# Kernel optimization log

Measured on AMD Instinct MI355X. Metric: run time of the kernel, lower is better.

The kernel has to match this reference:

```python
import jax, jax.numpy as jnp
import numpy as np

N = 50000          # num member nodes == num provider nodes
E = 800000         # provider->member bipartite edges (avg degree 16)
IN_M = 128; IN_P = 128; HID = 128; HEADS = 4; LAT = 64
NEG = 0.2          # leaky_relu negative slope (PyG GATConv default)


def gat_conv(x, src, dst, W, a_src, a_dst, b, heads, ch):
    """PyG-style GATConv (eval mode, concat heads). x:[N,F], src/dst:[Etot]."""
    n = x.shape[0]
    h = (x @ W).reshape(n, heads, ch)                       # [N,H,C]
    s = jnp.sum(h * a_src, axis=-1)                         # [N,H]
    d = jnp.sum(h * a_dst, axis=-1)                         # [N,H]
    e = jax.nn.leaky_relu(s[src] + d[dst], NEG)             # [Etot,H]
    # segment softmax over edges grouped by destination node
    m = jax.ops.segment_max(e, dst, num_segments=n)
    p = jnp.exp(e - m[dst])
    z = jax.ops.segment_sum(p, dst, num_segments=n)
    alpha = p / (z[dst] + 1e-16)                            # [Etot,H]
    out = jax.ops.segment_sum(h[src] * alpha[..., None], dst, num_segments=n)
    return out.reshape(n, heads * ch) + b


def setup_inputs() -> dict:
    key = jax.random.key(0)
    ks = jax.random.split(key, 24)
    gl = lambda k, shape, fan: (jax.random.normal(k, shape, jnp.float32) / np.sqrt(fan).astype(np.float32))
    return {
        "x_member": jax.random.normal(ks[0], (N, IN_M), jnp.float32),
        "x_provider": jax.random.normal(ks[1], (N, IN_P), jnp.float32),
        "edge_index": jax.random.randint(ks[2], (2, E), 0, N),
        "W1_m": gl(ks[3], (IN_M, HID), IN_M),
        "a_src1_m": gl(ks[4], (HEADS, HID // HEADS), HID // HEADS),
        "a_dst1_m": gl(ks[5], (HEADS, HID // HEADS), HID // HEADS),
        "b1_m": jnp.zeros((HID,), jnp.float32),
        "W2_m": gl(ks[6], (HID, LAT), HID),
        "a_src2_m": gl(ks[7], (1, LAT), LAT),
        "a_dst2_m": gl(ks[8], (1, LAT), LAT),
        "b2_m": jnp.zeros((LAT,), jnp.float32),
        "W1_p": gl(ks[9], (IN_P, HID), IN_P),
        "a_src1_p": gl(ks[10], (HEADS, HID // HEADS), HID // HEADS),
        "a_dst1_p": gl(ks[11], (HEADS, HID // HEADS), HID // HEADS),
        "b1_p": jnp.zeros((HID,), jnp.float32),
        "W2_p": gl(ks[12], (HID, LAT), HID),
        "a_src2_p": gl(ks[13], (1, LAT), LAT),
        "a_dst2_p": gl(ks[14], (1, LAT), LAT),
        "b2_p": jnp.zeros((LAT,), jnp.float32),
        "Wd_m": gl(ks[15], (LAT, IN_M), LAT),
        "bd_m": jnp.zeros((IN_M,), jnp.float32),
        "Wd_p": gl(ks[16], (LAT, IN_P), LAT),
        "bd_p": jnp.zeros((IN_P,), jnp.float32),
    }


def reference(x_member, x_provider, edge_index,
              W1_m, a_src1_m, a_dst1_m, b1_m, W2_m, a_src2_m, a_dst2_m, b2_m,
              W1_p, a_src1_p, a_dst1_p, b1_p, W2_p, a_src2_p, a_dst2_p, b2_p,
              Wd_m, bd_m, Wd_p, bd_p):
    prov, memb = edge_index[0], edge_index[1]
    loop = jnp.arange(N)
    # member graph: self loops + (provider -> member); provider graph: reverse
    m_src = jnp.concatenate([loop, prov]); m_dst = jnp.concatenate([loop, memb])
    p_src = jnp.concatenate([loop, memb]); p_dst = jnp.concatenate([loop, prov])

    xm = jax.nn.elu(gat_conv(x_member, m_src, m_dst, W1_m, a_src1_m, a_dst1_m, b1_m, HEADS, HID // HEADS))
    z_m = gat_conv(xm, m_src, m_dst, W2_m, a_src2_m, a_dst2_m, b2_m, 1, LAT)

    xp = jax.nn.elu(gat_conv(x_provider, p_src, p_dst, W1_p, a_src1_p, a_dst1_p, b1_p, HEADS, HID // HEADS))
    z_p = gat_conv(xp, p_src, p_dst, W2_p, a_src2_p, a_dst2_p, b2_p, 1, LAT)

    x_hat_member = z_m @ Wd_m + bd_m
    x_hat_provider = z_p @ Wd_p + bd_p
    edge_logits = jnp.sum(z_p[prov] * z_m[memb], axis=1)
    return (x_hat_member, x_hat_provider, edge_logits)
```

## Files before the change

kernel.cpp:

```cpp
#include <hip/hip_runtime.h>
#include <hip/hip_fp16.h>
#include <stdint.h>

__device__ __forceinline__ unsigned int pack_h2(float a, float b) {
    return (unsigned int)__half_as_ushort(__float2half(a)) |
           ((unsigned int)__half_as_ushort(__float2half(b)) << 16);
}
__device__ __forceinline__ float4 cvt_h4(uint2 r) {
    __half2 h0 = *reinterpret_cast<__half2*>(&r.x);
    __half2 h1 = *reinterpret_cast<__half2*>(&r.y);
    float2 f0 = __half22float2(h0), f1 = __half22float2(h1);
    return make_float4(f0.x, f0.y, f1.x, f1.y);
}

template<int K, int COUT, bool ADD_BIAS, bool IN_HALF, bool OUT_HALF>
__global__ __launch_bounds__(256) void gemm_kernel(const void* __restrict__ X0,
                                                   const void* __restrict__ X1,
                                                   const float* __restrict__ W0,
                                                   const float* __restrict__ W1,
                                                   const float* __restrict__ b0,
                                                   const float* __restrict__ b1,
                                                   void* __restrict__ out0,
                                                   void* __restrict__ out1, int n)
{
    constexpr int KC   = 64;
    constexpr int CPT  = (COUT >= 128) ? 8 : 4;
    constexpr int TX   = COUT / CPT;
    constexpr int TY   = 256 / TX;
    constexpr int ROWS = TY * 4;

    __shared__ float Wl[KC * COUT];
    __shared__ float Xl[KC * ROWS];

    const int side = blockIdx.y;
    const void*  Xv   = side ? X1 : X0;
    const float* W    = side ? W1 : W0;
    const float* bias = side ? b1 : b0;
    void* outp        = side ? out1 : out0;

    const int tid  = threadIdx.x;
    const int row0 = blockIdx.x * ROWS;
    const int tx = tid % TX, ty = tid / TX;
    const int c0 = tx * CPT;

    float acc[4][CPT];
    #pragma unroll
    for (int i = 0; i < 4; ++i)
        #pragma unroll
        for (int j = 0; j < CPT; ++j) acc[i][j] = 0.f;

    for (int k0 = 0; k0 < K; k0 += KC) {
        for (int i = tid; i < KC * COUT / 4; i += 256) {
            int e0 = i * 4;
            int r = e0 / COUT, c = e0 - r * COUT;
            reinterpret_cast<float4*>(Wl)[i] =
                *reinterpret_cast<const float4*>(W + (size_t)(k0 + r) * COUT + c);
        }
        for (int i = tid; i < ROWS * KC / 4; i += 256) {
            int r = i / (KC / 4), c4 = i - r * (KC / 4);
            int gr = row0 + r;
            float4 v = make_float4(0.f, 0.f, 0.f, 0.f);
            if (gr < n) {
                if constexpr (IN_HALF) {
                    const __half* X = (const __half*)Xv;
                    v = cvt_h4(*reinterpret_cast<const uint2*>(X + (size_t)gr * K + k0 + c4 * 4));
                } else {
                    const float* X = (const float*)Xv;
                    v = *reinterpret_cast<const float4*>(X + (size_t)gr * K + k0 + c4 * 4);
                }
            }
            int cb = c4 * 4;
            Xl[(cb + 0) * ROWS + r] = v.x;
            Xl[(cb + 1) * ROWS + r] = v.y;
            Xl[(cb + 2) * ROWS + r] = v.z;
            Xl[(cb + 3) * ROWS + r] = v.w;
        }
        __syncthreads();

        #pragma unroll 16
        for (int kk = 0; kk < KC; ++kk) {
            float b[CPT];
            #pragma unroll
            for (int j = 0; j < CPT; ++j) b[j] = Wl[kk * COUT + c0 + j];
            float4 a4 = *reinterpret_cast<const float4*>(Xl + kk * ROWS + ty * 4);
            float a[4] = {a4.x, a4.y, a4.z, a4.w};
            #pragma unroll
            for (int i = 0; i < 4; ++i)
                #pragma unroll
                for (int j = 0; j < CPT; ++j)
                    acc[i][j] = fmaf(a[i], b[j], acc[i][j]);
        }
        __syncthreads();
    }

    #pragma unroll
    for (int i = 0; i < 4; ++i) {
        int gr = row0 + ty * 4 + i;
        if (gr < n) {
            float v[CPT];
            #pragma unroll
            for (int j = 0; j < CPT; ++j) {
                v[j] = acc[i][j];
                if constexpr (ADD_BIAS) v[j] += bias[c0 + j];
            }
            if constexpr (OUT_HALF) {
                __half* po = (__half*)outp + (size_t)gr * COUT + c0;
                if constexpr (CPT == 8) {
                    uint4 w;
                    w.x = pack_h2(v[0], v[1]); w.y = pack_h2(v[2], v[3]);
                    w.z = pack_h2(v[4], v[5]); w.w = pack_h2(v[6], v[7]);
                    *reinterpret_cast<uint4*>(po) = w;
                } else {
                    uint2 w;
                    w.x = pack_h2(v[0], v[1]); w.y = pack_h2(v[2], v[3]);
                    *reinterpret_cast<uint2*>(po) = w;
                }
            } else {
                float* po = (float*)outp + (size_t)gr * COUT + c0;
                #pragma unroll
                for (int j = 0; j < CPT; ++j) po[j] = v[j];
            }
        }
    }
}

template<int C, int H>
__global__ __launch_bounds__(256) void sd_kernel(const __half* __restrict__ hm,
                                                 const __half* __restrict__ hp,
                                                 const float* __restrict__ as_m,
                                                 const float* __restrict__ ad_m,
                                                 const float* __restrict__ as_p,
                                                 const float* __restrict__ ad_p,
                                                 float* __restrict__ s,
                                                 float* __restrict__ d, int N)
{
    constexpr int CH = C / H;
    int t = blockIdx.x * 256 + threadIdx.x;
    if (t >= 2 * N * H) return;
    int node = t / H, hh = t - (t / H) * H;
    int side = node >= N;
    int lN = node - (side ? N : 0);
    const __half* hfp = (side ? hp : hm) + (size_t)lN * C + hh * CH;
    const float* as = (side ? as_p : as_m) + hh * CH;
    const float* ad = (side ? ad_p : ad_m) + hh * CH;
    float av = 0.f, dv = 0.f;
    #pragma unroll
    for (int c = 0; c < CH; ++c) {
        float hv = __half2float(hfp[c]);
        av = fmaf(hv, as[c], av);
        dv = fmaf(hv, ad[c], dv);
    }
    s[t] = av; d[t] = dv;
}

#define BSH 7
#define BCAP 2560
#define CHUNK_E 4096

__global__ __launch_bounds__(256) void bucket_scatter_kernel(const int* __restrict__ prov,
                                                             const int* __restrict__ memb,
                                                             int* __restrict__ bcnt,
                                                             int2* __restrict__ bstore,
                                                             int e, int n, int nbuck)
{
    __shared__ int hist[1024];
    __shared__ int lbase[1024];
    const int tid = threadIdx.x;
    const int e0 = blockIdx.x * CHUNK_E;
    const int e1 = min(e, e0 + CHUNK_E);

    for (int i = tid; i < nbuck; i += 256) hist[i] = 0;
    __syncthreads();
    for (int t = e0 + tid; t < e1; t += 256) {
        int m = memb[t], p = prov[t];
        atomicAdd(&hist[m >> BSH], 1);
        atomicAdd(&hist[(n + p) >> BSH], 1);
    }
    __syncthreads();
    for (int i = tid; i < nbuck; i += 256) {
        int h = hist[i];
        lbase[i] = (h > 0) ? atomicAdd(&bcnt[i], h) : 0;
        hist[i] = 0;
    }
    __syncthreads();
    for (int t = e0 + tid; t < e1; t += 256) {
        int m = memb[t], p = prov[t];
        int b1 = m >> BSH;
        int pos1 = lbase[b1] + atomicAdd(&hist[b1], 1);
        if (pos1 < BCAP) bstore[(size_t)b1 * BCAP + pos1] = make_int2(m, p);
        int d2 = n + p;
        int b2 = d2 >> BSH;
        int pos2 = lbase[b2] + atomicAdd(&hist[b2], 1);
        if (pos2 < BCAP) bstore[(size_t)b2 * BCAP + pos2] = make_int2(d2, m);
    }
}

__global__ __launch_bounds__(1024) void bucket_scan_kernel(const int* __restrict__ bcnt,
                                                           int* __restrict__ bbase,
                                                           int* __restrict__ roff,
                                                           int nb, int n2)
{
    __shared__ int tmp[1024];
    int tid = threadIdx.x;
    int v = (tid < nb) ? min(bcnt[tid], BCAP) : 0;
    tmp[tid] = v; __syncthreads();
    for (int o = 1; o < 1024; o <<= 1) {
        int x = (tid >= o) ? tmp[tid - o] : 0;
        __syncthreads();
        tmp[tid] += x;
        __syncthreads();
    }
    bbase[tid] = tmp[tid] - v;
    if (tid == 0) roff[n2] = tmp[1023];
}

__global__ __launch_bounds__(256) void bucket_build_kernel(const int* __restrict__ bcnt,
                                                           const int* __restrict__ bbase,
                                                           const int2* __restrict__ bstore,
                                                           int* __restrict__ roff,
                                                           int* __restrict__ colA,
                                                           int n2)
{
    __shared__ int2 ent[BCAP];
    __shared__ int  colL[BCAP];
    __shared__ int  cnts[128], pref[128], curs[128];

    const int b = blockIdx.x, tid = threadIdx.x;
    const int node0 = b << BSH;
    const int cnt  = min(bcnt[b], BCAP);
    const int base = bbase[b];

    if (tid < 128) cnts[tid] = 0;
    __syncthreads();
    for (int i = tid; i < cnt; i += 256) {
        int2 v = bstore[(size_t)b * BCAP + i];
        ent[i] = v;
        atomicAdd(&cnts[v.x - node0], 1);
    }
    __syncthreads();
    if (tid < 128) pref[tid] = cnts[tid];
    __syncthreads();
    #pragma unroll
    for (int o = 1; o < 128; o <<= 1) {
        int x = 0;
        if (tid < 128 && tid >= o) x = pref[tid - o];
        __syncthreads();
        if (tid < 128) pref[tid] += x;
        __syncthreads();
    }
    if (tid < 128) {
        int node = node0 + tid;
        if (node < n2) roff[node] = base + pref[tid] - cnts[tid];
        curs[tid] = 0;
    }
    __syncthreads();
    for (int i = tid; i < cnt; i += 256) {
        int2 v = ent[i];
        int loc = v.x - node0;
        int slot = (pref[loc] - cnts[loc]) + atomicAdd(&curs[loc], 1);
        colL[slot] = v.y;
    }
    __syncthreads();
    for (int i = tid; i < cnt; i += 256) colA[base + i] = colL[i];
}

template<int H>
__device__ __forceinline__ float selH(const float* arr, int hd) {
    float v = arr[0];
    #pragma unroll
    for (int hh = 1; hh < H; ++hh) v = (hd == hh) ? arr[hh] : v;
    return v;
}

template<int C, int H, bool ELU, bool OUTH>
__device__ __forceinline__ void agg_one_fullwave(int iG, int lN, int lane,
                                                 const __half* __restrict__ hf,
                                                 const float* __restrict__ sarr,
                                                 const float* __restrict__ sb,
                                                 const float* __restrict__ darr,
                                                 const int* __restrict__ roff,
                                                 const int* __restrict__ col,
                                                 const float* __restrict__ bias,
                                                 void* __restrict__ out,
                                                 float* alsW, int* srcsW)
{
    constexpr int CH = C / H;
    constexpr int LR = C / 4;
    constexpr int EP = 64 / LR;
    const int start = roff[iG], end = roff[iG + 1];
    const int deg = end - start;

    float dh[H], es[H];
    #pragma unroll
    for (int hh = 0; hh < H; ++hh) dh[hh] = darr[(size_t)iG * H + hh];
    #pragma unroll
    for (int hh = 0; hh < H; ++hh) {
        float e = sarr[(size_t)iG * H + hh] + dh[hh];
        es[hh] = fmaxf(e, 0.2f * e);
    }

    if (deg <= 64) {
        int srcL = (lane < deg) ? col[start + lane] : 0;
        float pl[H], zh[H];
        if (lane < deg) {
            #pragma unroll
            for (int hh = 0; hh < H; ++hh) {
                float e = sb[(size_t)srcL * H + hh] + dh[hh];
                pl[hh] = __expf(fmaxf(e, 0.2f * e));
            }
        } else {
            #pragma unroll
            for (int hh = 0; hh < H; ++hh) pl[hh] = 0.f;
        }
        #pragma unroll
        for (int hh = 0; hh < H; ++hh) zh[hh] = pl[hh];
        #pragma unroll
        for (int hh = 0; hh < H; ++hh)
            for (int o = 32; o >= 1; o >>= 1)
                zh[hh] += __shfl_xor(zh[hh], o, 64);
        if (lane < deg) srcsW[lane] = srcL;
        float aself[H];
        #pragma unroll
        for (int hh = 0; hh < H; ++hh) {
            float se = __expf(es[hh]);
            float invz = 1.f / (zh[hh] + se + 1e-16f);
            aself[hh] = se * invz;
            if (lane < deg) alsW[hh * 65 + lane] = pl[hh] * invz;
        }
        asm volatile("s_waitcnt lgkmcnt(0)" ::: "memory");

        const int sub = lane / LR;
        const int q   = lane % LR;
        const int c0  = q * 4;
        const int hd  = c0 / CH;

        float4 acc = make_float4(0.f, 0.f, 0.f, 0.f);
        if (sub == 0) {
            float4 hv = cvt_h4(*reinterpret_cast<const uint2*>(hf + (size_t)lN * C + c0));
            float a = selH<H>(aself, hd);
            acc.x = a * hv.x; acc.y = a * hv.y; acc.z = a * hv.z; acc.w = a * hv.w;
        }
        const float* alsB = alsW + hd * 65;
        int t = sub;
#define GSTEP(U)                                                                     \
        while (t + (U - 1) * EP < deg) {                                             \
            int ss[U]; float aa[U]; uint2 rr[U];                                     \
            _Pragma("unroll")                                                        \
            for (int u = 0; u < U; ++u) { ss[u] = srcsW[t + u * EP]; aa[u] = alsB[t + u * EP]; } \
            _Pragma("unroll")                                                        \
            for (int u = 0; u < U; ++u)                                              \
                rr[u] = *reinterpret_cast<const uint2*>(hf + (size_t)ss[u] * C + c0); \
            _Pragma("unroll")                                                        \
            for (int u = 0; u < U; ++u) {                                            \
                float4 hv = cvt_h4(rr[u]);                                           \
                acc.x = fmaf(aa[u], hv.x, acc.x);                                    \
                acc.y = fmaf(aa[u], hv.y, acc.y);                                    \
                acc.z = fmaf(aa[u], hv.z, acc.z);                                    \
                acc.w = fmaf(aa[u], hv.w, acc.w);                                    \
            }                                                                        \
            t += U * EP;                                                             \
        }
        GSTEP(8)
        GSTEP(4)
        GSTEP(2)
        GSTEP(1)
#undef GSTEP
        #pragma unroll
        for (int o = LR; o < 64; o <<= 1) {
            acc.x += __shfl_xor(acc.x, o, 64);
            acc.y += __shfl_xor(acc.y, o, 64);
            acc.z += __shfl_xor(acc.z, o, 64);
            acc.w += __shfl_xor(acc.w, o, 64);
        }
        if (sub == 0) {
            float4 bv = *reinterpret_cast<const float4*>(bias + c0);
            float4 v = make_float4(acc.x + bv.x, acc.y + bv.y, acc.z + bv.z, acc.w + bv.w);
            if constexpr (ELU) {
                v.x = (v.x > 0.f) ? v.x : (__expf(v.x) - 1.f);
                v.y = (v.y > 0.f) ? v.y : (__expf(v.y) - 1.f);
                v.z = (v.z > 0.f) ? v.z : (__expf(v.z) - 1.f);
                v.w = (v.w > 0.f) ? v.w : (__expf(v.w) - 1.f);
            }
            if constexpr (OUTH) {
                uint2 w; w.x = pack_h2(v.x, v.y); w.y = pack_h2(v.z, v.w);
                *reinterpret_cast<uint2*>((__half*)out + (size_t)lN * C + c0) = w;
            } else {
                *reinterpret_cast<float4*>((float*)out + (size_t)lN * C + c0) = v;
            }
        }
        return;
    }

    float zh[H];
    #pragma unroll
    for (int hh = 0; hh < H; ++hh) zh[hh] = 0.f;
    for (int base = start; base < end; base += 64) {
        int idx = base + lane;
        if (idx < end) {
            int src = col[idx];
            #pragma unroll
            for (int hh = 0; hh < H; ++hh) {
                float e = sb[(size_t)src * H + hh] + dh[hh];
                e = fmaxf(e, 0.2f * e);
                zh[hh] += __expf(e);
            }
        }
    }
    #pragma unroll
    for (int hh = 0; hh < H; ++hh) {
        for (int o = 32; o >= 1; o >>= 1) zh[hh] += __shfl_xor(zh[hh], o, 64);
        zh[hh] += __expf(es[hh]);
    }

    constexpr int CPL = C / 64;
    const int cc0 = lane * CPL;
    const int hdl = cc0 / CH;
    const float invz = 1.f / (zh[hdl] + 1e-16f);
    const float d_l  = dh[hdl];

    float acc2[CPL];
    {
        float aself = __expf(es[hdl]) * invz;
        #pragma unroll
        for (int j = 0; j < CPL; ++j) acc2[j] = aself * __half2float(hf[(size_t)lN * C + cc0 + j]);
    }
    for (int base = start; base < end; base += 64) {
        int idx = base + lane;
        int srcL2 = (idx < end) ? col[idx] : 0;
        int cnt2 = min(64, end - base);
        for (int t = 0; t < cnt2; ++t) {
            int st = __shfl(srcL2, t, 64);
            float e = sb[(size_t)st * H + hdl] + d_l;
            e = fmaxf(e, 0.2f * e);
            float a = __expf(e) * invz;
            #pragma unroll
            for (int j = 0; j < CPL; ++j)
                acc2[j] = fmaf(a, __half2float(hf[(size_t)st * C + cc0 + j]), acc2[j]);
        }
    }
    #pragma unroll
    for (int j = 0; j < CPL; ++j) {
        int c = cc0 + j;
        float v = acc2[j] + bias[c];
        if constexpr (ELU) v = (v > 0.f) ? v : (__expf(v) - 1.f);
        if constexpr (OUTH) ((__half*)out)[(size_t)lN * C + c] = __float2half(v);
        else                ((float*)out)[(size_t)lN * C + c] = v;
    }
}

template<int C, int H, bool ELU, bool OUTH>
__global__ __launch_bounds__(256) void agg_kernel(const __half* __restrict__ hm,
                                                  const __half* __restrict__ hp,
                                                  const float* __restrict__ sarr,
                                                  const float* __restrict__ darr,
                                                  const int* __restrict__ roff,
                                                  const int* __restrict__ col,
                                                  const float* __restrict__ bias_m,
                                                  const float* __restrict__ bias_p,
                                                  void* __restrict__ out_m,
                                                  void* __restrict__ out_p, int N)
{
    constexpr int CH  = C / H;
    constexpr int LRd = C / 8;
    constexpr int EPd = 32 / LRd;
    constexpr int H33 = H * 33;
    constexpr int ALSZ = (2 * H33 > H * 65) ? 2 * H33 : H * 65;
    __shared__ float als[4][ALSZ];
    __shared__ int   srcs[4][64];

    const int n2 = 2 * N;
    const int wslot = threadIdx.x >> 6;
    const int wv    = (blockIdx.x * 256 + threadIdx.x) >> 6;
    const int lane  = threadIdx.x & 63;
    const int g = lane >> 5, l = lane & 31;
    const int i0 = wv * 2;
    if (i0 >= n2) return;

    const bool nval = (i0 + g) < n2;
    const int iN = nval ? (i0 + g) : (n2 - 1);
    const int side = (iN >= N) ? 1 : 0;
    const int lN = iN - side * N;
    const __half* hf = side ? hp : hm;
    const float* sb = sarr + (size_t)side * N * H;
    const float* biasS = side ? bias_p : bias_m;
    void* outS = side ? out_p : out_m;

    const int start = roff[iN], end = roff[iN + 1];
    const int deg = nval ? (end - start) : 0;
    const int degO = __shfl_xor(deg, 32, 64);
    const int degm = max(deg, degO);

    if (degm <= 32) {
        float dh[H], es[H];
        if constexpr (H == 4) {
            float4 dv = *reinterpret_cast<const float4*>(darr + (size_t)iN * 4);
            float4 sv = *reinterpret_cast<const float4*>(sarr + (size_t)iN * 4);
            dh[0] = dv.x; dh[1] = dv.y; dh[2] = dv.z; dh[3] = dv.w;
            float ev[4] = {sv.x + dv.x, sv.y + dv.y, sv.z + dv.z, sv.w + dv.w};
            #pragma unroll
            for (int hh = 0; hh < 4; ++hh) es[hh] = fmaxf(ev[hh], 0.2f * ev[hh]);
        } else {
            #pragma unroll
            for (int hh = 0; hh < H; ++hh) {
                dh[hh] = darr[(size_t)iN * H + hh];
                float e = sarr[(size_t)iN * H + hh] + dh[hh];
                es[hh] = fmaxf(e, 0.2f * e);
            }
        }

        int srcL = (l < deg) ? col[start + l] : 0;
        float pl[H];
        if (l < deg) {
            if constexpr (H == 4) {
                float4 sv = *reinterpret_cast<const float4*>(sb + (size_t)srcL * 4);
                float ee[4] = {sv.x + dh[0], sv.y + dh[1], sv.z + dh[2], sv.w + dh[3]};
                #pragma unroll
                for (int hh = 0; hh < 4; ++hh) pl[hh] = __expf(fmaxf(ee[hh], 0.2f * ee[hh]));
            } else {
                #pragma unroll
                for (int hh = 0; hh < H; ++hh) {
                    float e = sb[(size_t)srcL * H + hh] + dh[hh];
                    pl[hh] = __expf(fmaxf(e, 0.2f * e));
                }
            }
        } else {
            #pragma unroll
            for (int hh = 0; hh < H; ++hh) pl[hh] = 0.f;
        }
        float zh[H];
        #pragma unroll
        for (int hh = 0; hh < H; ++hh) zh[hh] = pl[hh];
        #pragma unroll
        for (int hh = 0; hh < H; ++hh)
            #pragma unroll
            for (int o = 16; o >= 1; o >>= 1)
                zh[hh] += __shfl_xor(zh[hh], o, 64);
        if (l < deg) srcs[wslot][g * 32 + l] = srcL;
        float aself[H];
        #pragma unroll
        for (int hh = 0; hh < H; ++hh) {
            float se = __expf(es[hh]);
            float invz = 1.f / (zh[hh] + se + 1e-16f);
            aself[hh] = se * invz;
            if (l < deg) als[wslot][g * H33 + hh * 33 + l] = pl[hh] * invz;
        }
        asm volatile("s_waitcnt lgkmcnt(0)" ::: "memory");

        const int sub = l / LRd;
        const int q   = l % LRd;
        const int c0  = q * 8;
        const int hd  = c0 / CH;

        float acc[8];
        #pragma unroll
        for (int j = 0; j < 8; ++j) acc[j] = 0.f;
        if (sub == 0) {
            uint4 r = *reinterpret_cast<const uint4*>(hf + (size_t)lN * C + c0);
            float4 lo = cvt_h4(make_uint2(r.x, r.y));
            float4 hi = cvt_h4(make_uint2(r.z, r.w));
            float a = selH<H>(aself, hd);
            acc[0] = a * lo.x; acc[1] = a * lo.y; acc[2] = a * lo.z; acc[3] = a * lo.w;
            acc[4] = a * hi.x; acc[5] = a * hi.y; acc[6] = a * hi.z; acc[7] = a * hi.w;
        }
        const int*   srcB = &srcs[wslot][g * 32];
        const float* alsB = &als[wslot][g * H33 + hd * 33];
        int t = sub;
#define GSTEP(U)                                                                     \
        while (t + (U - 1) * EPd < deg) {                                            \
            int ss[U]; float aa[U]; uint4 rr[U];                                     \
            _Pragma("unroll")                                                        \
            for (int u = 0; u < U; ++u) { ss[u] = srcB[t + u * EPd]; aa[u] = alsB[t + u * EPd]; } \
            _Pragma("unroll")                                                        \
            for (int u = 0; u < U; ++u)                                              \
                rr[u] = *reinterpret_cast<const uint4*>(hf + (size_t)ss[u] * C + c0); \
            _Pragma("unroll")                                                        \
            for (int u = 0; u < U; ++u) {                                            \
                float4 lo = cvt_h4(make_uint2(rr[u].x, rr[u].y));                    \
                float4 hi = cvt_h4(make_uint2(rr[u].z, rr[u].w));                    \
                acc[0] = fmaf(aa[u], lo.x, acc[0]);                                  \
                acc[1] = fmaf(aa[u], lo.y, acc[1]);                                  \
                acc[2] = fmaf(aa[u], lo.z, acc[2]);                                  \
                acc[3] = fmaf(aa[u], lo.w, acc[3]);                                  \
                acc[4] = fmaf(aa[u], hi.x, acc[4]);                                  \
                acc[5] = fmaf(aa[u], hi.y, acc[5]);                                  \
                acc[6] = fmaf(aa[u], hi.z, acc[6]);                                  \
                acc[7] = fmaf(aa[u], hi.w, acc[7]);                                  \
            }                                                                        \
            t += U * EPd;                                                            \
        }
        GSTEP(4)
        GSTEP(2)
        GSTEP(1)
#undef GSTEP
        #pragma unroll
        for (int o = LRd; o < 32; o <<= 1) {
            #pragma unroll
            for (int j = 0; j < 8; ++j) acc[j] += __shfl_xor(acc[j], o, 64);
        }
        if (sub == 0 && nval) {
            float4 b0 = *reinterpret_cast<const float4*>(biasS + c0);
            float4 b1 = *reinterpret_cast<const float4*>(biasS + c0 + 4);
            float v[8] = {acc[0] + b0.x, acc[1] + b0.y, acc[2] + b0.z, acc[3] + b0.w,
                          acc[4] + b1.x, acc[5] + b1.y, acc[6] + b1.z, acc[7] + b1.w};
            if constexpr (ELU) {
                #pragma unroll
                for (int j = 0; j < 8; ++j) v[j] = (v[j] > 0.f) ? v[j] : (__expf(v[j]) - 1.f);
            }
            if constexpr (OUTH) {
                uint4 w;
                w.x = pack_h2(v[0], v[1]); w.y = pack_h2(v[2], v[3]);
                w.z = pack_h2(v[4], v[5]); w.w = pack_h2(v[6], v[7]);
                *reinterpret_cast<uint4*>((__half*)outS + (size_t)lN * C + c0) = w;
            } else {
                float* po = (float*)outS + (size_t)lN * C + c0;
                *reinterpret_cast<float4*>(po)     = make_float4(v[0], v[1], v[2], v[3]);
                *reinterpret_cast<float4*>(po + 4) = make_float4(v[4], v[5], v[6], v[7]);
            }
        }
        return;
    }

    for (int nd = 0; nd < 2; ++nd) {
        int i = i0 + nd;
        if (i >= n2) break;
        int sd2 = (i >= N) ? 1 : 0;
        int ln2 = i - sd2 * N;
        agg_one_fullwave<C, H, ELU, OUTH>(i, ln2, lane,
                                          sd2 ? hp : hm,
                                          sarr, sarr + (size_t)sd2 * N * H, darr,
                                          roff, col,
                                          sd2 ? bias_p : bias_m,
                                          sd2 ? out_p : out_m,
                                          als[wslot], srcs[wslot]);
    }
}

__global__ __launch_bounds__(256) void logits_kernel(const float* __restrict__ zp,
                                                     const float* __restrict__ zm,
                                                     const int* __restrict__ prov,
                                                     const int* __restrict__ memb,
                                                     float* __restrict__ outv, int e)
{
    const int nw   = (gridDim.x * 256) >> 6;
    const int wv   = (blockIdx.x * 256 + threadIdx.x) >> 6;
    const int lane = threadIdx.x & 63;
    const int g = lane >> 4, q = lane & 15;
    for (int base = wv * 8; base < e; base += nw * 8) {
        int e1 = base + g, e2 = base + 4 + g;
        bool v1 = e1 < e, v2 = e2 < e;
        int i1 = v1 ? e1 : (e - 1), i2 = v2 ? e2 : (e - 1);
        int p1 = prov[i1], m1 = memb[i1];
        int p2 = prov[i2], m2 = memb[i2];
        float4 a1 = *reinterpret_cast<const float4*>(zp + (size_t)p1 * 64 + q * 4);
        float4 b1 = *reinterpret_cast<const float4*>(zm + (size_t)m1 * 64 + q * 4);
        float4 a2 = *reinterpret_cast<const float4*>(zp + (size_t)p2 * 64 + q * 4);
        float4 b2 = *reinterpret_cast<const float4*>(zm + (size_t)m2 * 64 + q * 4);
        float s1 = a1.x * b1.x + a1.y * b1.y + a1.z * b1.z + a1.w * b1.w;
        float s2 = a2.x * b2.x + a2.y * b2.y + a2.z * b2.z + a2.w * b2.w;
        #pragma unroll
        for (int o = 1; o < 16; o <<= 1) {
            s1 += __shfl_xor(s1, o, 64);
            s2 += __shfl_xor(s2, o, 64);
        }
        if (q == 0) {
            if (v1) outv[e1] = s1;
            if (v2) outv[e2] = s2;
        }
    }
}

extern "C" void kernel_launch(void* const* d_in, const int* in_sizes, int n_in,
                              void* d_out, int out_size, void* d_ws, size_t ws_size,
                              hipStream_t stream)
{
    const int N_ = in_sizes[0] / 128;
    const int E_ = in_sizes[2] / 2;

    const float* x_member   = (const float*)d_in[0];
    const float* x_provider = (const float*)d_in[1];
    const int*   prov = (const int*)d_in[2];
    const int*   memb = prov + E_;
    const float* W1_m = (const float*)d_in[3];
    const float* a_src1_m = (const float*)d_in[4];
    const float* a_dst1_m = (const float*)d_in[5];
    const float* b1_m = (const float*)d_in[6];
    const float* W2_m = (const float*)d_in[7];
    const float* a_src2_m = (const float*)d_in[8];
    const float* a_dst2_m = (const float*)d_in[9];
    const float* b2_m = (const float*)d_in[10];
    const float* W1_p = (const float*)d_in[11];
    const float* a_src1_p = (const float*)d_in[12];
    const float* a_dst1_p = (const float*)d_in[13];
    const float* b1_p = (const float*)d_in[14];
    const float* W2_p = (const float*)d_in[15];
    const float* a_src2_p = (const float*)d_in[16];
    const float* a_dst2_p = (const float*)d_in[17];
    const float* b2_p = (const float*)d_in[18];
    const float* Wd_m = (const float*)d_in[19];
    const float* bd_m = (const float*)d_in[20];
    const float* Wd_p = (const float*)d_in[21];
    const float* bd_p = (const float*)d_in[22];

    const int n2 = 2 * N_;
    const int NB = (n2 + 127) >> BSH;

    char* p = (char*)d_ws;
    auto alloc = [&](size_t bytes) { void* q = (void*)p; p += (bytes + 255) & ~(size_t)255; return q; };
    __half* h1m   = (__half*)alloc((size_t)N_ * 128 * 2);
    __half* h1p   = (__half*)alloc((size_t)N_ * 128 * 2);
    __half* xm16m = (__half*)alloc((size_t)N_ * 128 * 2);
    __half* xm16p = (__half*)alloc((size_t)N_ * 128 * 2);
    float* zm     = (float*)alloc((size_t)N_ * 64 * 4);
    float* zp     = (float*)alloc((size_t)N_ * 64 * 4);
    float* s1     = (float*)alloc((size_t)n2 * 4 * 4);
    float* d1     = (float*)alloc((size_t)n2 * 4 * 4);
    float* s2     = (float*)alloc((size_t)n2 * 4);
    float* d2     = (float*)alloc((size_t)n2 * 4);
    int*   bcnt   = (int*)alloc((size_t)NB * 4);
    int*   bbase  = (int*)alloc(1024 * 4);
    int*   roff2  = (int*)alloc((size_t)(n2 + 1) * 4);
    int*   colA   = (int*)alloc((size_t)2 * E_ * 4);
    __half* h2m = h1m;
    __half* h2p = h1p;
    int2*  bstore = (int2*)h1m;

    hipMemsetAsync(bcnt, 0, (size_t)NB * 4, stream);
    bucket_scatter_kernel<<<(E_ + CHUNK_E - 1) / CHUNK_E, 256, 0, stream>>>(prov, memb, bcnt, bstore, E_, N_, NB);
    bucket_scan_kernel<<<1, 1024, 0, stream>>>(bcnt, bbase, roff2, NB, n2);
    bucket_build_kernel<<<NB, 256, 0, stream>>>(bcnt, bbase, bstore, roff2, colA, n2);

    const dim3 gg((N_ + 63) / 64, 2);

    gemm_kernel<128, 128, false, false, true><<<gg, 256, 0, stream>>>(
        x_member, x_provider, W1_m, W1_p, nullptr, nullptr, h1m, h1p, N_);
    sd_kernel<128, 4><<<(n2 * 4 + 255) / 256, 256, 0, stream>>>(
        h1m, h1p, a_src1_m, a_dst1_m, a_src1_p, a_dst1_p, s1, d1, N_);
    agg_kernel<128, 4, true, true><<<(n2 + 7) / 8, 256, 0, stream>>>(
        h1m, h1p, s1, d1, roff2, colA, b1_m, b1_p, xm16m, xm16p, N_);

    gemm_kernel<128, 64, false, true, true><<<gg, 256, 0, stream>>>(
        xm16m, xm16p, W2_m, W2_p, nullptr, nullptr, h2m, h2p, N_);
    sd_kernel<64, 1><<<(n2 + 255) / 256, 256, 0, stream>>>(
        h2m, h2p, a_src2_m, a_dst2_m, a_src2_p, a_dst2_p, s2, d2, N_);
    agg_kernel<64, 1, false, false><<<(n2 + 7) / 8, 256, 0, stream>>>(
        h2m, h2p, s2, d2, roff2, colA, b2_m, b2_p, zm, zp, N_);

    float* out = (float*)d_out;
    gemm_kernel<64, 128, true, false, false><<<gg, 256, 0, stream>>>(
        zm, zp, Wd_m, Wd_p, bd_m, bd_p, out, out + (size_t)N_ * 128, N_);
    logits_kernel<<<2048, 256, 0, stream>>>(zp, zm, prov, memb, out + (size_t)N_ * 128 * 2, E_);
}
```

Baseline: 513.9 us.

## Fuse attention score dots into GEMM epilogue and store latent z in fp16

Computes the per-node source and destination attention scores inside the GEMM epilogue using a lane shuffle reduction, and removes the two separate sd_kernel launches along with their re-read of h. The second-layer aggregation now writes z in fp16, which the decoder GEMM and the edge logits kernel read with half-width loads. An 8-wide unrolled gather step is also added to the aggregation loop. The fp16 z lowers precision of the outputs and logits, and the epilogue adds shuffles to the GEMM.

```diff
diff --git a/kernel.cpp b/kernel.cpp
--- a/kernel.cpp
+++ b/kernel.cpp
@@ -13,13 +13,19 @@
     return make_float4(f0.x, f0.y, f1.x, f1.y);
 }
 
-template<int K, int COUT, bool ADD_BIAS, bool IN_HALF, bool OUT_HALF>
+template<int K, int COUT, bool ADD_BIAS, bool IN_HALF, bool OUT_HALF, int SDH>
 __global__ __launch_bounds__(256) void gemm_kernel(const void* __restrict__ X0,
                                                    const void* __restrict__ X1,
                                                    const float* __restrict__ W0,
                                                    const float* __restrict__ W1,
                                                    const float* __restrict__ b0,
                                                    const float* __restrict__ b1,
+                                                   const float* __restrict__ as0,
+                                                   const float* __restrict__ ad0,
+                                                   const float* __restrict__ as1,
+                                                   const float* __restrict__ ad1,
+                                                   float* __restrict__ s_out,
+                                                   float* __restrict__ d_out,
                                                    void* __restrict__ out0,
                                                    void* __restrict__ out1, int n)
 {
@@ -93,6 +99,17 @@
         __syncthreads();
     }
 
+    float ascr[CPT], adtr[CPT];
+    int hd = 0;
+    if constexpr (SDH > 0) {
+        constexpr int CHh = COUT / SDH;
+        hd = c0 / CHh;
+        const float* asc = (side ? as1 : as0) + c0;
+        const float* adt = (side ? ad1 : ad0) + c0;
+        #pragma unroll
+        for (int j = 0; j < CPT; ++j) { ascr[j] = asc[j]; adtr[j] = adt[j]; }
+    }
+
     #pragma unroll
     for (int i = 0; i < 4; ++i) {
         int gr = row0 + ty * 4 + i;
@@ -102,6 +119,25 @@
             for (int j = 0; j < CPT; ++j) {
                 v[j] = acc[i][j];
                 if constexpr (ADD_BIAS) v[j] += bias[c0 + j];
+            }
+            if constexpr (SDH > 0) {
+                constexpr int CHh = COUT / SDH;
+                constexpr int GL = CHh / CPT;
+                float ps = 0.f, pd = 0.f;
+                #pragma unroll
+                for (int j = 0; j < CPT; ++j) {
+                    ps = fmaf(v[j], ascr[j], ps);
+                    pd = fmaf(v[j], adtr[j], pd);
+                }
+                #pragma unroll
+                for (int o = 1; o < GL; o <<= 1) {
+                    ps += __shfl_xor(ps, o, 64);
+                    pd += __shfl_xor(pd, o, 64);
+                }
+                if ((tx % GL) == 0) {
+                    size_t gi = (size_t)(side ? n + gr : gr) * SDH + hd;
+                    s_out[gi] = ps; d_out[gi] = pd;
+                }
             }
             if constexpr (OUT_HALF) {
                 __half* po = (__half*)outp + (size_t)gr * COUT + c0;
@@ -122,35 +158,6 @@
             }
         }
     }
-}
-
-template<int C, int H>
-__global__ __launch_bounds__(256) void sd_kernel(const __half* __restrict__ hm,
-                                                 const __half* __restrict__ hp,
-                                                 const float* __restrict__ as_m,
-                                                 const float* __restrict__ ad_m,
-                                                 const float* __restrict__ as_p,
-                                                 const float* __restrict__ ad_p,
-                                                 float* __restrict__ s,
-                                                 float* __restrict__ d, int N)
-{
-    constexpr int CH = C / H;
-    int t = blockIdx.x * 256 + threadIdx.x;
-    if (t >= 2 * N * H) return;
-    int node = t / H, hh = t - (t / H) * H;
-    int side = node >= N;
-    int lN = node - (side ? N : 0);
-    const __half* hfp = (side ? hp : hm) + (size_t)lN * C + hh * CH;
-    const float* as = (side ? as_p : as_m) + hh * CH;
-    const float* ad = (side ? ad_p : ad_m) + hh * CH;
-    float av = 0.f, dv = 0.f;
-    #pragma unroll
-    for (int c = 0; c < CH; ++c) {
-        float hv = __half2float(hfp[c]);
-        av = fmaf(hv, as[c], av);
-        dv = fmaf(hv, ad[c], dv);
-    }
-    s[t] = av; d[t] = dv;
 }
 
 #define BSH 7
@@ -588,6 +595,7 @@
             }                                                                        \
             t += U * EPd;                                                            \
         }
+        GSTEP(8)
         GSTEP(4)
         GSTEP(2)
         GSTEP(1)
@@ -635,8 +643,8 @@
     }
 }
 
-__global__ __launch_bounds__(256) void logits_kernel(const float* __restrict__ zp,
-                                                     const float* __restrict__ zm,
+__global__ __launch_bounds__(256) void logits_kernel(const __half* __restrict__ zp,
+                                                     const __half* __restrict__ zm,
                                                      const int* __restrict__ prov,
                                                      const int* __restrict__ memb,
                                                      float* __restrict__ outv, int e)
@@ -644,21 +652,28 @@
     const int nw   = (gridDim.x * 256) >> 6;
     const int wv   = (blockIdx.x * 256 + threadIdx.x) >> 6;
     const int lane = threadIdx.x & 63;
-    const int g = lane >> 4, q = lane & 15;
-    for (int base = wv * 8; base < e; base += nw * 8) {
-        int e1 = base + g, e2 = base + 4 + g;
+    const int g = lane >> 3, q = lane & 7;
+    const int c0 = q * 8;
+    for (int base = wv * 16; base < e; base += nw * 16) {
+        int e1 = base + g, e2 = base + 8 + g;
         bool v1 = e1 < e, v2 = e2 < e;
         int i1 = v1 ? e1 : (e - 1), i2 = v2 ? e2 : (e - 1);
         int p1 = prov[i1], m1 = memb[i1];
         int p2 = prov[i2], m2 = memb[i2];
-        float4 a1 = *reinterpret_cast<const float4*>(zp + (size_t)p1 * 64 + q * 4);
-        float4 b1 = *reinterpret_cast<const float4*>(zm + (size_t)m1 * 64 + q * 4);
-        float4 a2 = *reinterpret_cast<const float4*>(zp + (size_t)p2 * 64 + q * 4);
-        float4 b2 = *reinterpret_cast<const float4*>(zm + (size_t)m2 * 64 + q * 4);
-        float s1 = a1.x * b1.x + a1.y * b1.y + a1.z * b1.z + a1.w * b1.w;
-        float s2 = a2.x * b2.x + a2.y * b2.y + a2.z * b2.z + a2.w * b2.w;
-        #pragma unroll
-        for (int o = 1; o < 16; o <<= 1) {
+        uint4 a1 = *reinterpret_cast<const uint4*>(zp + (size_t)p1 * 64 + c0);
+        uint4 b1 = *reinterpret_cast<const uint4*>(zm + (size_t)m1 * 64 + c0);
+        uint4 a2 = *reinterpret_cast<const uint4*>(zp + (size_t)p2 * 64 + c0);
+        uint4 b2 = *reinterpret_cast<const uint4*>(zm + (size_t)m2 * 64 + c0);
+        float4 al1 = cvt_h4(make_uint2(a1.x, a1.y)), ah1 = cvt_h4(make_uint2(a1.z, a1.w));
+        float4 bl1 = cvt_h4(make_uint2(b1.x, b1.y)), bh1 = cvt_h4(make_uint2(b1.z, b1.w));
+        float4 al2 = cvt_h4(make_uint2(a2.x, a2.y)), ah2 = cvt_h4(make_uint2(a2.z, a2.w));
+        float4 bl2 = cvt_h4(make_uint2(b2.x, b2.y)), bh2 = cvt_h4(make_uint2(b2.z, b2.w));
+        float s1 = al1.x * bl1.x + al1.y * bl1.y + al1.z * bl1.z + al1.w * bl1.w
+                 + ah1.x * bh1.x + ah1.y * bh1.y + ah1.z * bh1.z + ah1.w * bh1.w;
+        float s2 = al2.x * bl2.x + al2.y * bl2.y + al2.z * bl2.z + al2.w * bl2.w
+                 + ah2.x * bh2.x + ah2.y * bh2.y + ah2.z * bh2.z + ah2.w * bh2.w;
+        #pragma unroll
+        for (int o = 1; o < 8; o <<= 1) {
             s1 += __shfl_xor(s1, o, 64);
             s2 += __shfl_xor(s2, o, 64);
         }
@@ -710,8 +725,8 @@
     __half* h1p   = (__half*)alloc((size_t)N_ * 128 * 2);
     __half* xm16m = (__half*)alloc((size_t)N_ * 128 * 2);
     __half* xm16p = (__half*)alloc((size_t)N_ * 128 * 2);
-    float* zm     = (float*)alloc((size_t)N_ * 64 * 4);
-    float* zp     = (float*)alloc((size_t)N_ * 64 * 4);
+    __half* zm16  = (__half*)alloc((size_t)N_ * 64 * 2);
+    __half* zp16  = (__half*)alloc((size_t)N_ * 64 * 2);
     float* s1     = (float*)alloc((size_t)n2 * 4 * 4);
     float* d1     = (float*)alloc((size_t)n2 * 4 * 4);
     float* s2     = (float*)alloc((size_t)n2 * 4);
@@ -730,23 +745,23 @@
     bucket_build_kernel<<<NB, 256, 0, stream>>>(bcnt, bbase, bstore, roff2, colA, n2);
 
     const dim3 gg((N_ + 63) / 64, 2);
-
-    gemm_kernel<128, 128, false, false, true><<<gg, 256, 0, stream>>>(
-        x_member, x_provider, W1_m, W1_p, nullptr, nullptr, h1m, h1p, N_);
-    sd_kernel<128, 4><<<(n2 * 4 + 255) / 256, 256, 0, stream>>>(
-        h1m, h1p, a_src1_m, a_dst1_m, a_src1_p, a_dst1_p, s1, d1, N_);
+    float* out = (float*)d_out;
+
+    gemm_kernel<128, 128, false, false, true, 4><<<gg, 256, 0, stream>>>(
+        x_member, x_provider, W1_m, W1_p, nullptr, nullptr,
+        a_src1_m, a_dst1_m, a_src1_p, a_dst1_p, s1, d1, h1m, h1p, N_);
     agg_kernel<128, 4, true, true><<<(n2 + 7) / 8, 256, 0, stream>>>(
         h1m, h1p, s1, d1, roff2, colA, b1_m, b1_p, xm16m, xm16p, N_);
 
-    gemm_kernel<128, 64, false, true, true><<<gg, 256, 0, stream>>>(
-        xm16m, xm16p, W2_m, W2_p, nullptr, nullptr, h2m, h2p, N_);
-    sd_kernel<64, 1><<<(n2 + 255) / 256, 256, 0, stream>>>(
-        h2m, h2p, a_src2_m, a_dst2_m, a_src2_p, a_dst2_p, s2, d2, N_);
-    agg_kernel<64, 1, false, false><<<(n2 + 7) / 8, 256, 0, stream>>>(
-        h2m, h2p, s2, d2, roff2, colA, b2_m, b2_p, zm, zp, N_);
-
-    float* out = (float*)d_out;
-    gemm_kernel<64, 128, true, false, false><<<gg, 256, 0, stream>>>(
-        zm, zp, Wd_m, Wd_p, bd_m, bd_p, out, out + (size_t)N_ * 128, N_);
-    logits_kernel<<<2048, 256, 0, stream>>>(zp, zm, prov, memb, out + (size_t)N_ * 128 * 2, E_);
-}
+    gemm_kernel<128, 64, false, true, true, 1><<<gg, 256, 0, stream>>>(
+        xm16m, xm16p, W2_m, W2_p, nullptr, nullptr,
+        a_src2_m, a_dst2_m, a_src2_p, a_dst2_p, s2, d2, h2m, h2p, N_);
+    agg_kernel<64, 1, false, true><<<(n2 + 7) / 8, 256, 0, stream>>>(
+        h2m, h2p, s2, d2, roff2, colA, b2_m, b2_p, zm16, zp16, N_);
+
+    gemm_kernel<64, 128, true, true, false, 0><<<gg, 256, 0, stream>>>(
+        zm16, zp16, Wd_m, Wd_p, bd_m, bd_p,
+        nullptr, nullptr, nullptr, nullptr, nullptr, nullptr,
+        out, out + (size_t)N_ * 128, N_);
+    logits_kernel<<<2048, 256, 0, stream>>>(zp16, zm16, prov, memb, out + (size_t)N_ * 128 * 2, E_);
+}
```

After: 483.1 us. 1.06x faster.
